# Optimization experiments

Hardware: AMD Instinct MI355X
Metric: run time of the kernel (lower is better)

The kernel has to match this reference:

```python
import jax, jax.numpy as jnp
import numpy as np

IN_C = 31
OUT_C = 31
GRID = 5          # grid_size
K = 3             # spline_order
NUM_BASIS = GRID + K                  # 8 B-spline basis functions
COEF_LEN = IN_C * OUT_C * NUM_BASIS   # 7688
UW_LEN = IN_C * OUT_C                 # 961 (univariate_weight)
RW_LEN = IN_C * OUT_C                 # 961 (residual_weight)
PNUM = COEF_LEN + UW_LEN + RW_LEN     # 9610 = kan_params_num


def _ext_grid():
    # uniform grid on grid_range=(-1,1), extended by K knots on each side
    h = 2.0 / GRID
    return jnp.arange(-K, GRID + K + 1, dtype=jnp.float32) * h - 1.0  # (GRID+2K+1,)


def bspline_basis(x):
    # x: (N, IN_C) -> (N, IN_C, NUM_BASIS) via Cox-de Boor recursion
    grid = _ext_grid()
    xx = x[..., None]
    b = ((xx >= grid[:-1]) & (xx < grid[1:])).astype(x.dtype)
    for p in range(1, K + 1):
        left = (xx - grid[: -(p + 1)]) / (grid[p:-1] - grid[: -(p + 1)]) * b[..., :-1]
        right = (grid[p + 1:] - xx) / (grid[p + 1:] - grid[1:-p]) * b[..., 1:]
        b = left + right
    return b


def setup_inputs() -> dict:
    key = jax.random.key(0)
    k1, k2, k3 = jax.random.split(key, 3)
    x = jax.random.normal(k1, (1, IN_C, 128, 128), jnp.float32)
    # HyperspectralGeneratorLayer: per-pixel (1x1 conv) map in_channels -> kan_params_num
    gen_w = jax.random.normal(k2, (PNUM, IN_C), jnp.float32) * 0.02
    gen_b = jax.random.normal(k3, (PNUM,), jnp.float32) * 0.02
    return {"x": x, "gen_w": gen_w, "gen_b": gen_b}


def reference(x, gen_w, gen_b):
    B, C, H, W = x.shape
    xf = x.transpose(0, 2, 3, 1).reshape(B * H * W, C)      # (N, 31)
    # generator: per-pixel KAN parameter vector (N, 9610)
    w = xf @ gen_w.T + gen_b
    coef = w[:, :COEF_LEN].reshape(-1, IN_C, OUT_C, NUM_BASIS)
    uw = w[:, COEF_LEN:COEF_LEN + UW_LEN].reshape(-1, IN_C, OUT_C)
    rw = w[:, COEF_LEN + UW_LEN:].reshape(-1, IN_C, OUT_C)
    # per-pixel KAN: phi_ij(x_i) = uw_ij * spline_ij(x_i) + rw_ij * silu(x_i); y_j = sum_i phi_ij
    basis = bspline_basis(xf)                               # (N, 31, 8)
    spline = jnp.einsum('nik,niok->nio', basis, coef)       # (N, 31, 31)
    y = jnp.einsum('nio,nio->no', spline, uw) \
        + jnp.einsum('ni,nio->no', jax.nn.silu(xf), rw)     # (N, 31)
    return y.reshape(B, H, W, OUT_C).transpose(0, 3, 1, 2)
```

## Files before the change

kernel.cpp:

```cpp
#include <hip/hip_runtime.h>
#include <hip/hip_bf16.h>
#include <math.h>

#define IN_C 31
#define OUT_C 31
#define NPIX 16384
#define UW_OFF 7688
#define RW_OFF 8649
#define PART_OFF (640 * 1024)
#define CHUNK_BYTES 20480

typedef __attribute__((ext_vector_type(8))) _Float16 f16x8;
typedef __attribute__((ext_vector_type(4))) float f32x4;

__device__ inline short f2h(float f) {
    union { _Float16 h; short s; } cv;
    cv.h = (_Float16)f;
    return cv.s;
}

__global__ __launch_bounds__(64) void kan_prep_kernel(
    const float* __restrict__ gw, const float* __restrict__ gb,
    unsigned short* __restrict__ ws)
{
    const int blk = blockIdx.x;
    const int i   = blk / 20;
    const int ch  = blk % 20;
    const int l   = threadIdx.x;
    const int col = l & 15;
    const int krow = l >> 4;
    const int o = (ch & 1) * 16 + col;

    int p;
    if (ch < 16)      p = (i * 31 + o) * 8 + (ch >> 1);
    else if (ch < 18) p = UW_OFF + i * 31 + o;
    else              p = RW_OFF + i * 31 + o;

    short v8[8];
#pragma unroll
    for (int j = 0; j < 8; ++j) {
        const int c = krow * 8 + j;
        float v = 0.f;
        if (o < OUT_C) v = (c < IN_C) ? gw[p * 31 + c] : gb[p];
        v8[j] = f2h(v);
    }
    *(f16x8*)&ws[(blk * 64 + l) * 8] = *(f16x8*)v8;
}

__device__ __forceinline__ void stage_i(const unsigned char* wsrc,
                                        unsigned char* ldst, int t) {
#pragma unroll
    for (int k = 0; k < 2; ++k) {
        const int off = (k * 512 + t) * 16;
        __builtin_amdgcn_global_load_lds(
            (const __attribute__((address_space(1))) unsigned int*)(wsrc + off),
            (__attribute__((address_space(3))) unsigned int*)(ldst + off),
            16, 0, 0);
    }
    if (t < 256) {
        const int off = (1024 + t) * 16;
        __builtin_amdgcn_global_load_lds(
            (const __attribute__((address_space(1))) unsigned int*)(wsrc + off),
            (__attribute__((address_space(3))) unsigned int*)(ldst + off),
            16, 0, 0);
    }
}

__global__ __launch_bounds__(512) void kan_mfma11_kernel(
    const float* __restrict__ x,
    const unsigned char* __restrict__ wsw,
    float* __restrict__ parts,
    float* __restrict__ out,
    int nsplit)
{
    const int t = threadIdx.x;
    const int l = t & 63;
    const int w = t >> 6;
    const int pix0 = blockIdx.x * 128;
    const int csize = (IN_C + nsplit - 1) / nsplit;
    const int ibase = blockIdx.y * csize;
    const int iend = min(ibase + csize, IN_C);

    __shared__ __align__(16) unsigned char bufs[4][CHUNK_BYTES];

    const int n0 = w * 16;
    const int prow = pix0 + n0 + (l & 15);

    f16x8 xv8f;
    {
        const int cb = (l >> 4) * 8;
#pragma unroll
        for (int j = 0; j < 8; ++j) {
            const int c = cb + j;
            const float v = (c < IN_C) ? x[c * NPIX + prow] : 1.0f;
            xv8f[j] = (_Float16)v;
        }
    }

    f32x4 Y[2];
    Y[0] = (f32x4){0.f, 0.f, 0.f, 0.f};
    Y[1] = (f32x4){0.f, 0.f, 0.f, 0.f};

    stage_i(wsw + (size_t)ibase * CHUNK_BYTES, bufs[0], t);
    if (ibase + 1 < iend)
        stage_i(wsw + (size_t)(ibase + 1) * CHUNK_BYTES, bufs[1], t);
    __syncthreads();

    const int npairs = (iend - ibase + 1) >> 1;

#pragma unroll 1
    for (int tp = 0; tp < npairs; ++tp) {
        const int i0 = ibase + 2 * tp;
        const bool has1 = (i0 + 1) < iend;

        if (tp + 1 < npairs) {
            const int nx = i0 + 2;
            unsigned char* d0 = bufs[2 * ((tp + 1) & 1)];
            stage_i(wsw + (size_t)nx * CHUNK_BYTES, d0, t);
            if (nx + 1 < iend)
                stage_i(wsw + (size_t)(nx + 1) * CHUNK_BYTES, d0 + CHUNK_BYTES, t);
        }

        const float xa = x[i0 * NPIX + prow];
        const float xb = has1 ? x[(i0 + 1) * NPIX + prow] : 0.f;

        _Float16 basA[8], basB[8];
        f16x8 arwA, arwB;
#pragma unroll
        for (int s = 0; s < 2; ++s) {
            const float xv = (s == 0) ? xa : xb;
            const float tb = (xv + 2.2f) * 2.5f;
            const float jf = floorf(tb);
            const float u  = tb - jf;
            const int  jj  = (int)jf;
            const float u2 = u * u, u3 = u2 * u;
            const float b0v = u3 * (1.f / 6.f);
            const float b1v = (-3.f * u3 + 3.f * u2 + 3.f * u + 1.f) * (1.f / 6.f);
            const float b2v = (3.f * u3 - 6.f * u2 + 4.f) * (1.f / 6.f);
            const float omu = 1.f - u;
            const float b3v = omu * omu * omu * (1.f / 6.f);
#pragma unroll
            for (int m = 0; m < 8; ++m) {
                const int d = jj - m;
                const float bv = (d == 0) ? b0v : (d == 1) ? b1v : (d == 2) ? b2v
                               : (d == 3) ? b3v : 0.f;
                if (s == 0) basA[m] = (_Float16)bv; else basB[m] = (_Float16)bv;
            }
            const float sil = xv / (1.f + __expf(-xv));
            if (s == 0) arwA = xv8f * (_Float16)sil;
            else        arwB = xv8f * (_Float16)sil;
        }

        const unsigned char* wbA = bufs[2 * (tp & 1)];
        const unsigned char* wbB = wbA + CHUNK_BYTES;

        f32x4 SPA[2], UWA[2], SPB[2], UWB[2];
#pragma unroll
        for (int nt = 0; nt < 2; ++nt) {
            SPA[nt] = (f32x4){0.f, 0.f, 0.f, 0.f};
            UWA[nt] = (f32x4){0.f, 0.f, 0.f, 0.f};
            SPB[nt] = (f32x4){0.f, 0.f, 0.f, 0.f};
            UWB[nt] = (f32x4){0.f, 0.f, 0.f, 0.f};
        }

#pragma unroll
        for (int p = 0; p < 10; ++p) {
            const f16x8 a0 = *(const f16x8*)(wbA + ((p * 2 + 0) * 64 + l) * 16);
            const f16x8 a1 = *(const f16x8*)(wbA + ((p * 2 + 1) * 64 + l) * 16);
            const f16x8 c0 = *(const f16x8*)(wbB + ((p * 2 + 0) * 64 + l) * 16);
            const f16x8 c1 = *(const f16x8*)(wbB + ((p * 2 + 1) * 64 + l) * 16);
            if (p < 8) {
                const f16x8 afA = xv8f * basA[p];
                SPA[0] = __builtin_amdgcn_mfma_f32_16x16x32_f16(afA, a0, SPA[0], 0, 0, 0);
                SPA[1] = __builtin_amdgcn_mfma_f32_16x16x32_f16(afA, a1, SPA[1], 0, 0, 0);
                if (has1) {
                    const f16x8 afB = xv8f * basB[p];
                    SPB[0] = __builtin_amdgcn_mfma_f32_16x16x32_f16(afB, c0, SPB[0], 0, 0, 0);
                    SPB[1] = __builtin_amdgcn_mfma_f32_16x16x32_f16(afB, c1, SPB[1], 0, 0, 0);
                }
            } else if (p == 8) {
                UWA[0] = __builtin_amdgcn_mfma_f32_16x16x32_f16(xv8f, a0, UWA[0], 0, 0, 0);
                UWA[1] = __builtin_amdgcn_mfma_f32_16x16x32_f16(xv8f, a1, UWA[1], 0, 0, 0);
                if (has1) {
                    UWB[0] = __builtin_amdgcn_mfma_f32_16x16x32_f16(xv8f, c0, UWB[0], 0, 0, 0);
                    UWB[1] = __builtin_amdgcn_mfma_f32_16x16x32_f16(xv8f, c1, UWB[1], 0, 0, 0);
                }
            } else {
                Y[0] = __builtin_amdgcn_mfma_f32_16x16x32_f16(arwA, a0, Y[0], 0, 0, 0);
                Y[1] = __builtin_amdgcn_mfma_f32_16x16x32_f16(arwA, a1, Y[1], 0, 0, 0);
                if (has1) {
                    Y[0] = __builtin_amdgcn_mfma_f32_16x16x32_f16(arwB, c0, Y[0], 0, 0, 0);
                    Y[1] = __builtin_amdgcn_mfma_f32_16x16x32_f16(arwB, c1, Y[1], 0, 0, 0);
                }
            }
        }

#pragma unroll
        for (int nt = 0; nt < 2; ++nt)
#pragma unroll
            for (int r = 0; r < 4; ++r) {
                Y[nt][r] = fmaf(UWA[nt][r], SPA[nt][r], Y[nt][r]);
                if (has1) Y[nt][r] = fmaf(UWB[nt][r], SPB[nt][r], Y[nt][r]);
            }

        __syncthreads();
    }

    float* yb = (float*)bufs;
#pragma unroll
    for (int nt = 0; nt < 2; ++nt)
#pragma unroll
        for (int r = 0; r < 4; ++r) {
            const int p = n0 + (l >> 4) * 4 + r;
            const int o = nt * 16 + (l & 15);
            if (o < OUT_C) yb[p * 33 + o] = Y[nt][r];
        }
    __syncthreads();

    float* dst = (blockIdx.y == 0) ? out
               : (parts + (size_t)(blockIdx.y - 1) * OUT_C * NPIX);
    for (int idx = t; idx < 128 * OUT_C; idx += 512) {
        const int n = idx & 127, o = idx >> 7;
        dst[o * NPIX + pix0 + n] = yb[n * 33 + o];
    }
}

__global__ __launch_bounds__(256) void kan_combine_kernel(
    float* __restrict__ out, const float* __restrict__ parts, int npart)
{
    const int e = blockIdx.x * 256 + threadIdx.x;
    const int nv = (OUT_C * NPIX) / 4;
    if (e < nv) {
        f32x4 a = ((const f32x4*)out)[e];
        for (int j = 0; j < npart; ++j)
            a += ((const f32x4*)parts)[e + (size_t)j * nv];
        ((f32x4*)out)[e] = a;
    }
}

extern "C" void kernel_launch(void* const* d_in, const int* in_sizes, int n_in,
                              void* d_out, int out_size, void* d_ws, size_t ws_size,
                              hipStream_t stream) {
    const float* x  = (const float*)d_in[0];
    const float* gw = (const float*)d_in[1];
    const float* gb = (const float*)d_in[2];
    float* out = (float*)d_out;
    unsigned short* ws = (unsigned short*)d_ws;
    float* parts = (float*)((char*)d_ws + PART_OFF);

    const size_t part_bytes = (size_t)OUT_C * NPIX * 4;
    int nsplit = 4;
    if (ws_size < PART_OFF + 3 * part_bytes) nsplit = 2;

    hipLaunchKernelGGL(kan_prep_kernel, dim3(620), dim3(64), 0, stream, gw, gb, ws);
    hipLaunchKernelGGL(kan_mfma11_kernel, dim3(NPIX / 128, nsplit), dim3(512), 0, stream,
                       x, (const unsigned char*)d_ws, parts, out, nsplit);
    const int nv = (OUT_C * NPIX) / 4;
    hipLaunchKernelGGL(kan_combine_kernel, dim3((nv + 255) / 256), dim3(256), 0, stream,
                       out, parts, nsplit - 1);
}
```

Measured before the change: 39.56 us.

## Split input channels eightfold and unroll the per-block loop into two staged pairs

Raises the input-channel split from 4 to 8, so each block handles 4 channels and the grid has twice as many blocks. The per-block loop becomes two fixed compute2 calls over two LDS buffers, which halves shared-memory use per block. The intent is more blocks resident per CU and better latency hiding. The cost is that prefetch overlap is lost, since each stage is synchronous, and the combine kernel must read 7 partial buffers instead of 3, adding global traffic. The kernel now assumes exactly 4 channels per block, so the nsplit=4 and nsplit=2 fallbacks for small workspaces would compute wrong results.

```diff
diff --git a/kernel.cpp b/kernel.cpp
--- a/kernel.cpp
+++ b/kernel.cpp
@@ -66,7 +66,91 @@
     }
 }
 
-__global__ __launch_bounds__(512) void kan_mfma11_kernel(
+__device__ __forceinline__ void compute2(
+    int iA, const unsigned char* wbA, bool hasB, int iB, const unsigned char* wbB,
+    const float* __restrict__ x, int pr0, f16x8 xv8f, f32x4 Y[2], int l)
+{
+    const float xa = x[iA * NPIX + pr0];
+    const float xb = hasB ? x[iB * NPIX + pr0] : 0.f;
+
+    _Float16 basA[8], basB[8];
+    f16x8 arwA, arwB;
+#pragma unroll
+    for (int s = 0; s < 2; ++s) {
+        const float xv = (s == 0) ? xa : xb;
+        const float tb = (xv + 2.2f) * 2.5f;
+        const float jf = floorf(tb);
+        const float u  = tb - jf;
+        const int  jj  = (int)jf;
+        const float u2 = u * u, u3 = u2 * u;
+        const float b0v = u3 * (1.f / 6.f);
+        const float b1v = (-3.f * u3 + 3.f * u2 + 3.f * u + 1.f) * (1.f / 6.f);
+        const float b2v = (3.f * u3 - 6.f * u2 + 4.f) * (1.f / 6.f);
+        const float omu = 1.f - u;
+        const float b3v = omu * omu * omu * (1.f / 6.f);
+#pragma unroll
+        for (int m = 0; m < 8; ++m) {
+            const int d = jj - m;
+            const float bv = (d == 0) ? b0v : (d == 1) ? b1v : (d == 2) ? b2v
+                           : (d == 3) ? b3v : 0.f;
+            if (s == 0) basA[m] = (_Float16)bv; else basB[m] = (_Float16)bv;
+        }
+        const float sil = xv / (1.f + __expf(-xv));
+        if (s == 0) arwA = xv8f * (_Float16)sil;
+        else        arwB = xv8f * (_Float16)sil;
+    }
+
+    f32x4 SPA[2], UWA[2], SPB[2], UWB[2];
+#pragma unroll
+    for (int nt = 0; nt < 2; ++nt) {
+        SPA[nt] = (f32x4){0.f, 0.f, 0.f, 0.f};
+        UWA[nt] = (f32x4){0.f, 0.f, 0.f, 0.f};
+        SPB[nt] = (f32x4){0.f, 0.f, 0.f, 0.f};
+        UWB[nt] = (f32x4){0.f, 0.f, 0.f, 0.f};
+    }
+
+#pragma unroll
+    for (int p = 0; p < 10; ++p) {
+        const f16x8 a0 = *(const f16x8*)(wbA + ((p * 2 + 0) * 64 + l) * 16);
+        const f16x8 a1 = *(const f16x8*)(wbA + ((p * 2 + 1) * 64 + l) * 16);
+        const f16x8 c0 = *(const f16x8*)(wbB + ((p * 2 + 0) * 64 + l) * 16);
+        const f16x8 c1 = *(const f16x8*)(wbB + ((p * 2 + 1) * 64 + l) * 16);
+        if (p < 8) {
+            const f16x8 afA = xv8f * basA[p];
+            SPA[0] = __builtin_amdgcn_mfma_f32_16x16x32_f16(afA, a0, SPA[0], 0, 0, 0);
+            SPA[1] = __builtin_amdgcn_mfma_f32_16x16x32_f16(afA, a1, SPA[1], 0, 0, 0);
+            if (hasB) {
+                const f16x8 afB = xv8f * basB[p];
+                SPB[0] = __builtin_amdgcn_mfma_f32_16x16x32_f16(afB, c0, SPB[0], 0, 0, 0);
+                SPB[1] = __builtin_amdgcn_mfma_f32_16x16x32_f16(afB, c1, SPB[1], 0, 0, 0);
+            }
+        } else if (p == 8) {
+            UWA[0] = __builtin_amdgcn_mfma_f32_16x16x32_f16(xv8f, a0, UWA[0], 0, 0, 0);
+            UWA[1] = __builtin_amdgcn_mfma_f32_16x16x32_f16(xv8f, a1, UWA[1], 0, 0, 0);
+            if (hasB) {
+                UWB[0] = __builtin_amdgcn_mfma_f32_16x16x32_f16(xv8f, c0, UWB[0], 0, 0, 0);
+                UWB[1] = __builtin_amdgcn_mfma_f32_16x16x32_f16(xv8f, c1, UWB[1], 0, 0, 0);
+            }
+        } else {
+            Y[0] = __builtin_amdgcn_mfma_f32_16x16x32_f16(arwA, a0, Y[0], 0, 0, 0);
+            Y[1] = __builtin_amdgcn_mfma_f32_16x16x32_f16(arwA, a1, Y[1], 0, 0, 0);
+            if (hasB) {
+                Y[0] = __builtin_amdgcn_mfma_f32_16x16x32_f16(arwB, c0, Y[0], 0, 0, 0);
+                Y[1] = __builtin_amdgcn_mfma_f32_16x16x32_f16(arwB, c1, Y[1], 0, 0, 0);
+            }
+        }
+    }
+
+#pragma unroll
+    for (int nt = 0; nt < 2; ++nt)
+#pragma unroll
+        for (int r = 0; r < 4; ++r) {
+            Y[nt][r] = fmaf(UWA[nt][r], SPA[nt][r], Y[nt][r]);
+            if (hasB) Y[nt][r] = fmaf(UWB[nt][r], SPB[nt][r], Y[nt][r]);
+        }
+}
+
+__global__ __launch_bounds__(512) void kan_mfma14_kernel(
     const float* __restrict__ x,
     const unsigned char* __restrict__ wsw,
     float* __restrict__ parts,
@@ -81,10 +165,13 @@
     const int ibase = blockIdx.y * csize;
     const int iend = min(ibase + csize, IN_C);
 
-    __shared__ __align__(16) unsigned char bufs[4][CHUNK_BYTES];
+    __shared__ __align__(16) unsigned char bufs[2][CHUNK_BYTES];
 
     const int n0 = w * 16;
-    const int prow = pix0 + n0 + (l & 15);
+    const int pr0 = pix0 + n0 + (l & 15);
+
+    stage_i(wsw + (size_t)ibase * CHUNK_BYTES, bufs[0], t);
+    stage_i(wsw + (size_t)(ibase + 1) * CHUNK_BYTES, bufs[1], t);
 
     f16x8 xv8f;
     {
@@ -92,7 +179,7 @@
 #pragma unroll
         for (int j = 0; j < 8; ++j) {
             const int c = cb + j;
-            const float v = (c < IN_C) ? x[c * NPIX + prow] : 1.0f;
+            const float v = (c < IN_C) ? x[c * NPIX + pr0] : 1.0f;
             xv8f[j] = (_Float16)v;
         }
     }
@@ -101,111 +188,22 @@
     Y[0] = (f32x4){0.f, 0.f, 0.f, 0.f};
     Y[1] = (f32x4){0.f, 0.f, 0.f, 0.f};
 
-    stage_i(wsw + (size_t)ibase * CHUNK_BYTES, bufs[0], t);
-    if (ibase + 1 < iend)
-        stage_i(wsw + (size_t)(ibase + 1) * CHUNK_BYTES, bufs[1], t);
-    __syncthreads();
-
-    const int npairs = (iend - ibase + 1) >> 1;
-
-#pragma unroll 1
-    for (int tp = 0; tp < npairs; ++tp) {
-        const int i0 = ibase + 2 * tp;
-        const bool has1 = (i0 + 1) < iend;
-
-        if (tp + 1 < npairs) {
-            const int nx = i0 + 2;
-            unsigned char* d0 = bufs[2 * ((tp + 1) & 1)];
-            stage_i(wsw + (size_t)nx * CHUNK_BYTES, d0, t);
-            if (nx + 1 < iend)
-                stage_i(wsw + (size_t)(nx + 1) * CHUNK_BYTES, d0 + CHUNK_BYTES, t);
-        }
-
-        const float xa = x[i0 * NPIX + prow];
-        const float xb = has1 ? x[(i0 + 1) * NPIX + prow] : 0.f;
-
-        _Float16 basA[8], basB[8];
-        f16x8 arwA, arwB;
-#pragma unroll
-        for (int s = 0; s < 2; ++s) {
-            const float xv = (s == 0) ? xa : xb;
-            const float tb = (xv + 2.2f) * 2.5f;
-            const float jf = floorf(tb);
-            const float u  = tb - jf;
-            const int  jj  = (int)jf;
-            const float u2 = u * u, u3 = u2 * u;
-            const float b0v = u3 * (1.f / 6.f);
-            const float b1v = (-3.f * u3 + 3.f * u2 + 3.f * u + 1.f) * (1.f / 6.f);
-            const float b2v = (3.f * u3 - 6.f * u2 + 4.f) * (1.f / 6.f);
-            const float omu = 1.f - u;
-            const float b3v = omu * omu * omu * (1.f / 6.f);
-#pragma unroll
-            for (int m = 0; m < 8; ++m) {
-                const int d = jj - m;
-                const float bv = (d == 0) ? b0v : (d == 1) ? b1v : (d == 2) ? b2v
-                               : (d == 3) ? b3v : 0.f;
-                if (s == 0) basA[m] = (_Float16)bv; else basB[m] = (_Float16)bv;
-            }
-            const float sil = xv / (1.f + __expf(-xv));
-            if (s == 0) arwA = xv8f * (_Float16)sil;
-            else        arwB = xv8f * (_Float16)sil;
-        }
-
-        const unsigned char* wbA = bufs[2 * (tp & 1)];
-        const unsigned char* wbB = wbA + CHUNK_BYTES;
-
-        f32x4 SPA[2], UWA[2], SPB[2], UWB[2];
-#pragma unroll
-        for (int nt = 0; nt < 2; ++nt) {
-            SPA[nt] = (f32x4){0.f, 0.f, 0.f, 0.f};
-            UWA[nt] = (f32x4){0.f, 0.f, 0.f, 0.f};
-            SPB[nt] = (f32x4){0.f, 0.f, 0.f, 0.f};
-            UWB[nt] = (f32x4){0.f, 0.f, 0.f, 0.f};
-        }
-
-#pragma unroll
-        for (int p = 0; p < 10; ++p) {
-            const f16x8 a0 = *(const f16x8*)(wbA + ((p * 2 + 0) * 64 + l) * 16);
-            const f16x8 a1 = *(const f16x8*)(wbA + ((p * 2 + 1) * 64 + l) * 16);
-            const f16x8 c0 = *(const f16x8*)(wbB + ((p * 2 + 0) * 64 + l) * 16);
-            const f16x8 c1 = *(const f16x8*)(wbB + ((p * 2 + 1) * 64 + l) * 16);
-            if (p < 8) {
-                const f16x8 afA = xv8f * basA[p];
-                SPA[0] = __builtin_amdgcn_mfma_f32_16x16x32_f16(afA, a0, SPA[0], 0, 0, 0);
-                SPA[1] = __builtin_amdgcn_mfma_f32_16x16x32_f16(afA, a1, SPA[1], 0, 0, 0);
-                if (has1) {
-                    const f16x8 afB = xv8f * basB[p];
-                    SPB[0] = __builtin_amdgcn_mfma_f32_16x16x32_f16(afB, c0, SPB[0], 0, 0, 0);
-                    SPB[1] = __builtin_amdgcn_mfma_f32_16x16x32_f16(afB, c1, SPB[1], 0, 0, 0);
-                }
-            } else if (p == 8) {
-                UWA[0] = __builtin_amdgcn_mfma_f32_16x16x32_f16(xv8f, a0, UWA[0], 0, 0, 0);
-                UWA[1] = __builtin_amdgcn_mfma_f32_16x16x32_f16(xv8f, a1, UWA[1], 0, 0, 0);
-                if (has1) {
-                    UWB[0] = __builtin_amdgcn_mfma_f32_16x16x32_f16(xv8f, c0, UWB[0], 0, 0, 0);
-                    UWB[1] = __builtin_amdgcn_mfma_f32_16x16x32_f16(xv8f, c1, UWB[1], 0, 0, 0);
-                }
-            } else {
-                Y[0] = __builtin_amdgcn_mfma_f32_16x16x32_f16(arwA, a0, Y[0], 0, 0, 0);
-                Y[1] = __builtin_amdgcn_mfma_f32_16x16x32_f16(arwA, a1, Y[1], 0, 0, 0);
-                if (has1) {
-                    Y[0] = __builtin_amdgcn_mfma_f32_16x16x32_f16(arwB, c0, Y[0], 0, 0, 0);
-                    Y[1] = __builtin_amdgcn_mfma_f32_16x16x32_f16(arwB, c1, Y[1], 0, 0, 0);
-                }
-            }
-        }
-
-#pragma unroll
-        for (int nt = 0; nt < 2; ++nt)
-#pragma unroll
-            for (int r = 0; r < 4; ++r) {
-                Y[nt][r] = fmaf(UWA[nt][r], SPA[nt][r], Y[nt][r]);
-                if (has1) Y[nt][r] = fmaf(UWB[nt][r], SPB[nt][r], Y[nt][r]);
-            }
-
-        __syncthreads();
-    }
-
+    __syncthreads();
+
+    compute2(ibase, bufs[0], true, ibase + 1, bufs[1], x, pr0, xv8f, Y, l);
+
+    __syncthreads();
+
+    const bool has3 = (ibase + 3) < iend;
+    stage_i(wsw + (size_t)(ibase + 2) * CHUNK_BYTES, bufs[0], t);
+    if (has3)
+        stage_i(wsw + (size_t)(ibase + 3) * CHUNK_BYTES, bufs[1], t);
+
+    __syncthreads();
+
+    compute2(ibase + 2, bufs[0], has3, ibase + 3, bufs[1], x, pr0, xv8f, Y, l);
+
+    __syncthreads();
     float* yb = (float*)bufs;
 #pragma unroll
     for (int nt = 0; nt < 2; ++nt)
@@ -249,11 +247,12 @@
     float* parts = (float*)((char*)d_ws + PART_OFF);
 
     const size_t part_bytes = (size_t)OUT_C * NPIX * 4;
-    int nsplit = 4;
+    int nsplit = 8;
+    if (ws_size < PART_OFF + 7 * part_bytes) nsplit = 4;
     if (ws_size < PART_OFF + 3 * part_bytes) nsplit = 2;
 
     hipLaunchKernelGGL(kan_prep_kernel, dim3(620), dim3(64), 0, stream, gw, gb, ws);
-    hipLaunchKernelGGL(kan_mfma11_kernel, dim3(NPIX / 128, nsplit), dim3(512), 0, stream,
+    hipLaunchKernelGGL(kan_mfma14_kernel, dim3(NPIX / 128, nsplit), dim3(512), 0, stream,
                        x, (const unsigned char*)d_ws, parts, out, nsplit);
     const int nv = (OUT_C * NPIX) / 4;
     hipLaunchKernelGGL(kan_combine_kernel, dim3((nv + 255) / 256), dim3(256), 0, stream,
```

New measurement: 41.99 us. 1.06x slower.
